# Kernel tuning notes

Measured on AMD Instinct MI355X. Metric: run time of the kernel, lower is better.

Reference implementation:

```python
import jax, jax.numpy as jnp
import numpy as np

N = 32768   # total nodes
P = 1024    # nodes per graph
B = 32      # graphs (N = B*P)
D = 256     # dim_h
H = 8       # num_heads
E = 262144  # edges
BN_EPS = 1e-5


def setup_inputs() -> dict:
    key = jax.random.key(0)
    ks = jax.random.split(key, 24)
    s = 0.05
    x = jax.random.normal(ks[0], (N, D), jnp.float32)
    src = jax.random.randint(ks[1], (E,), 0, N, dtype=jnp.int32)
    dst = (src // P) * P + jax.random.randint(ks[2], (E,), 0, P, dtype=jnp.int32)
    edge_index = jnp.stack([src, dst])  # [2, E], edges within the same graph
    edge_attr = jax.random.normal(ks[3], (E, D), jnp.float32)
    return {
        "x": x,
        "edge_index": edge_index,
        "edge_attr": edge_attr,
        # GINE nn: Linear(D,D) -> ReLU -> Linear(D,D)
        "gin_w1": s * jax.random.normal(ks[4], (D, D)),
        "gin_b1": jnp.zeros((D,)),
        "gin_w2": s * jax.random.normal(ks[5], (D, D)),
        "gin_b2": jnp.zeros((D,)),
        # MultiheadAttention packed in-proj and out-proj
        "in_w": s * jax.random.normal(ks[6], (3 * D, D)),
        "in_b": jnp.zeros((3 * D,)),
        "out_w": s * jax.random.normal(ks[7], (D, D)),
        "out_b": jnp.zeros((D,)),
        # BatchNorm1d affine params (training-mode batch stats)
        "bn1l_g": jnp.ones((D,)) + s * jax.random.normal(ks[8], (D,)),
        "bn1l_b": s * jax.random.normal(ks[9], (D,)),
        "bn1a_g": jnp.ones((D,)) + s * jax.random.normal(ks[10], (D,)),
        "bn1a_b": s * jax.random.normal(ks[11], (D,)),
        # FF block: Linear(D,2D) -> ReLU -> Linear(2D,D)
        "ff_w1": s * jax.random.normal(ks[12], (2 * D, D)),
        "ff_b1": jnp.zeros((2 * D,)),
        "ff_w2": s * jax.random.normal(ks[13], (D, 2 * D)),
        "ff_b2": jnp.zeros((D,)),
        "bn2_g": jnp.ones((D,)) + s * jax.random.normal(ks[14], (D,)),
        "bn2_b": s * jax.random.normal(ks[15], (D,)),
    }


def _batchnorm(x, g, b):
    # BatchNorm1d, training mode: biased batch statistics over the node axis.
    m = jnp.mean(x, axis=0)
    v = jnp.mean((x - m) ** 2, axis=0)
    return g * (x - m) * jax.lax.rsqrt(v + BN_EPS) + b


def reference(x, edge_index, edge_attr, gin_w1, gin_b1, gin_w2, gin_b2,
              in_w, in_b, out_w, out_b, bn1l_g, bn1l_b, bn1a_g, bn1a_b,
              ff_w1, ff_b1, ff_w2, ff_b2, bn2_g, bn2_b):
    h_in = x
    # ---- local branch: GINEConv (eps = 0) ----
    msg = jax.nn.relu(x[edge_index[0]] + edge_attr)          # [E, D]
    aggr = jax.ops.segment_sum(msg, edge_index[1], num_segments=N)
    z = x + aggr                                             # (1+eps)*x_i + sum msg
    h_local = jax.nn.relu(z @ gin_w1.T + gin_b1) @ gin_w2.T + gin_b2
    h_local = _batchnorm(h_in + h_local, bn1l_g, bn1l_b)
    # ---- global branch: dense-batch MHA (equal-size graphs -> full mask) ----
    hd = x.reshape(B, P, D)
    qkv = hd @ in_w.T + in_b                                 # [B, P, 3D]
    q, k, v = jnp.split(qkv, 3, axis=-1)
    dh = D // H
    q = q.reshape(B, P, H, dh).transpose(0, 2, 1, 3)         # [B, H, P, dh]
    k = k.reshape(B, P, H, dh).transpose(0, 2, 1, 3)
    v = v.reshape(B, P, H, dh).transpose(0, 2, 1, 3)
    scores = jnp.einsum("bhqd,bhkd->bhqk", q, k) / np.sqrt(dh)
    attn = jax.nn.softmax(scores, axis=-1)
    o = jnp.einsum("bhqk,bhkd->bhqd", attn, v)               # [B, H, P, dh]
    o = o.transpose(0, 2, 1, 3).reshape(B, P, D) @ out_w.T + out_b
    h_attn = o.reshape(N, D)
    h_attn = _batchnorm(h_in + h_attn, bn1a_g, bn1a_b)
    # ---- combine + FF + norm ----
    h = h_local + h_attn
    ff = jax.nn.relu(h @ ff_w1.T + ff_b1) @ ff_w2.T + ff_b2
    h = _batchnorm(h + ff, bn2_g, bn2_b)
    return h
```

## Files before the change

### kernel.cpp

```cpp
#include <hip/hip_runtime.h>
#include <hip/hip_bf16.h>

constexpr int D = 256;
constexpr int PG = 1024;

typedef __attribute__((ext_vector_type(8))) short bf16x8;
typedef __attribute__((ext_vector_type(4))) float f32x4;

__device__ inline short f2bf(float f) {
    __hip_bfloat16 h = __float2bfloat16(f);
    return *reinterpret_cast<short*>(&h);
}
__device__ inline float bf2f(short s) {
    return __uint_as_float(((unsigned)(unsigned short)s) << 16);
}

__global__ __launch_bounds__(256) void cvt_weights(
    const float* __restrict__ w1, const float* __restrict__ w2,
    const float* __restrict__ w3, const float* __restrict__ w4,
    const float* __restrict__ w5, const float* __restrict__ w6,
    short* __restrict__ out)
{
    int i = blockIdx.x * 256 + threadIdx.x;
    const float* src; int base;
    if (i < 16384)      { if (i < 8192) { src = w1; base = 0; }
                          else          { src = w2; base = 8192; } }
    else if (i < 40960) { src = w3; base = 16384; }
    else if (i < 49152) { src = w4; base = 40960; }
    else if (i < 65536) { src = w5; base = 49152; }
    else                { src = w6; base = 65536; }
    int k = i - base;
    float4 a = ((const float4*)src)[k * 2];
    float4 b = ((const float4*)src)[k * 2 + 1];
    bf16x8 v;
    v[0] = f2bf(a.x); v[1] = f2bf(a.y); v[2] = f2bf(a.z); v[3] = f2bf(a.w);
    v[4] = f2bf(b.x); v[5] = f2bf(b.y); v[6] = f2bf(b.z); v[7] = f2bf(b.w);
    ((bf16x8*)out)[i] = v;
}

__global__ __launch_bounds__(256) void hist_kernel(
    const int* __restrict__ dst, int* __restrict__ cnt, int E)
{
    int e = blockIdx.x * 256 + threadIdx.x;
    if (e < E) atomicAdd(&cnt[dst[e]], 1);
}

__global__ __launch_bounds__(256) void scan_block(
    const int* __restrict__ cnt, int* __restrict__ excl, int* __restrict__ bsum)
{
    __shared__ int sm[256];
    const int t = threadIdx.x;
    const int i = blockIdx.x * 256 + t;
    int v = cnt[i];
    sm[t] = v;
    __syncthreads();
    #pragma unroll
    for (int o = 1; o < 256; o <<= 1) {
        int u = (t >= o) ? sm[t - o] : 0;
        __syncthreads();
        sm[t] += u;
        __syncthreads();
    }
    excl[i] = sm[t] - v;
    if (t == 255) bsum[blockIdx.x] = sm[255];
}

__global__ __launch_bounds__(128) void scan_bsum(int* __restrict__ bsum)
{
    __shared__ int sm[128];
    const int t = threadIdx.x;
    int v = bsum[t];
    sm[t] = v;
    __syncthreads();
    #pragma unroll
    for (int o = 1; o < 128; o <<= 1) {
        int u = (t >= o) ? sm[t - o] : 0;
        __syncthreads();
        sm[t] += u;
        __syncthreads();
    }
    bsum[t] = sm[t] - v;
}

__global__ __launch_bounds__(256) void scan_add(
    const int* __restrict__ excl, const int* __restrict__ bsum,
    int* __restrict__ rowptr, int* __restrict__ ofs)
{
    int i = blockIdx.x * 256 + threadIdx.x;
    int r = excl[i] + bsum[blockIdx.x];
    rowptr[i] = r;
    ofs[i] = r;
}

__global__ __launch_bounds__(256) void scatter_kernel(
    const int* __restrict__ src, const int* __restrict__ dst,
    int* __restrict__ ofs, int* __restrict__ eord, int* __restrict__ esrc, int E)
{
    int e = blockIdx.x * 256 + threadIdx.x;
    if (e >= E) return;
    int d = dst[e];
    int pos = atomicAdd(&ofs[d], 1);
    eord[pos] = e;
    esrc[pos] = src[e];
}

__global__ __launch_bounds__(256) void csr_aggr(
    const float* __restrict__ x, const float* __restrict__ ea,
    const int* __restrict__ rowptr, const int* __restrict__ cnt,
    const int* __restrict__ eord, const int* __restrict__ esrc,
    short* __restrict__ z)
{
    int gid = blockIdx.x * 256 + threadIdx.x;
    int node = gid >> 6;
    int c = (gid & 63) << 2;
    int start = rowptr[node];
    int deg = cnt[node];
    float4 acc = *(const float4*)(x + (size_t)node * D + c);
    for (int i = 0; i < deg; ++i) {
        int e = eord[start + i];
        int s = esrc[start + i];
        float4 xa = *(const float4*)(x + (size_t)s * D + c);
        float4 av = *(const float4*)(ea + (size_t)e * D + c);
        acc.x += fmaxf(xa.x + av.x, 0.f);
        acc.y += fmaxf(xa.y + av.y, 0.f);
        acc.z += fmaxf(xa.z + av.z, 0.f);
        acc.w += fmaxf(xa.w + av.w, 0.f);
    }
    short4 r;
    r.x = f2bf(acc.x); r.y = f2bf(acc.y); r.z = f2bf(acc.z); r.w = f2bf(acc.w);
    *(short4*)(z + (size_t)node * D + c) = r;
}

template<bool XF32, bool RELU, bool ADDF, bool ADDB, bool STATS, bool SCALEQ>
__global__ __launch_bounds__(256) void gemm_mfma(
    const short* __restrict__ X, const float* __restrict__ Xf,
    const short* __restrict__ W, const float* __restrict__ bias,
    const float* __restrict__ addf, const short* __restrict__ addb,
    short* __restrict__ Y, float* __restrict__ st, int K, int M)
{
    __shared__ __align__(16) short Xs[128 * 72];
    __shared__ __align__(16) short Ws[128 * 72];

    const int nbx = gridDim.x;
    const int nwg = nbx * gridDim.y;
    const int bid = blockIdx.y * nbx + blockIdx.x;
    const int cpx = nwg >> 3;
    const int wg  = (bid & 7) * cpx + (bid >> 3);
    const int r0 = (wg / nbx) * 128;
    const int c0 = (wg % nbx) * 128;

    const int t = threadIdx.x, w = t >> 6, l = t & 63;
    const int wr = w >> 1, wc = w & 1, lg = l >> 4, lm = l & 15;
    const int srow = t >> 3;
    const int scol = (t & 7) * 8;

    f32x4 acc[4][4];
    #pragma unroll
    for (int i = 0; i < 4; ++i)
        #pragma unroll
        for (int j = 0; j < 4; ++j)
            acc[i][j] = (f32x4){0.f, 0.f, 0.f, 0.f};

    for (int k0 = 0; k0 < K; k0 += 64) {
        __syncthreads();
        #pragma unroll
        for (int it = 0; it < 4; ++it) {
            int r = it * 32 + srow;
            bf16x8 xv;
            if (XF32) {
                const float* p = Xf + (size_t)(r0 + r) * K + k0 + scol;
                float4 a = *(const float4*)p;
                float4 b = *(const float4*)(p + 4);
                xv[0] = f2bf(a.x); xv[1] = f2bf(a.y); xv[2] = f2bf(a.z); xv[3] = f2bf(a.w);
                xv[4] = f2bf(b.x); xv[5] = f2bf(b.y); xv[6] = f2bf(b.z); xv[7] = f2bf(b.w);
            } else {
                xv = *(const bf16x8*)(X + (size_t)(r0 + r) * K + k0 + scol);
            }
            bf16x8 wv = *(const bf16x8*)(W + (size_t)(c0 + r) * K + k0 + scol);
            *(bf16x8*)&Xs[r * 72 + scol] = xv;
            *(bf16x8*)&Ws[r * 72 + scol] = wv;
        }
        __syncthreads();

        bf16x8 af[4][2], bfr[4][2];
        #pragma unroll
        for (int i = 0; i < 4; ++i)
            #pragma unroll
            for (int ks = 0; ks < 2; ++ks) {
                af[i][ks]  = *(const bf16x8*)&Xs[(wr*64 + i*16 + lm)*72 + ks*32 + lg*8];
                bfr[i][ks] = *(const bf16x8*)&Ws[(wc*64 + i*16 + lm)*72 + ks*32 + lg*8];
            }
        #pragma unroll
        for (int i = 0; i < 4; ++i)
            #pragma unroll
            for (int j = 0; j < 4; ++j) {
                acc[i][j] = __builtin_amdgcn_mfma_f32_16x16x32_bf16(af[i][0], bfr[j][0], acc[i][j], 0, 0, 0);
                acc[i][j] = __builtin_amdgcn_mfma_f32_16x16x32_bf16(af[i][1], bfr[j][1], acc[i][j], 0, 0, 0);
            }
    }

    float s4[4] = {}, q4[4] = {};
    #pragma unroll
    for (int j = 0; j < 4; ++j) {
        int col = c0 + wc*64 + j*16 + lm;
        float bj = bias[col];
        #pragma unroll
        for (int i = 0; i < 4; ++i) {
            #pragma unroll
            for (int r = 0; r < 4; ++r) {
                int row = r0 + wr*64 + i*16 + lg*4 + r;
                size_t off = (size_t)row * M + col;
                float v = acc[i][j][r] + bj;
                if (RELU) v = fmaxf(v, 0.f);
                if (SCALEQ) { if (col < 256) v *= 0.17677669529663687f; }
                if (ADDF) v += addf[off];
                if (ADDB) v += bf2f(addb[off]);
                if (STATS) { s4[j] += v; q4[j] = fmaf(v, v, q4[j]); }
                Y[off] = f2bf(v);
            }
        }
    }
    if (STATS) {
        #pragma unroll
        for (int j = 0; j < 4; ++j) {
            s4[j] += __shfl_xor(s4[j], 16); q4[j] += __shfl_xor(q4[j], 16);
            s4[j] += __shfl_xor(s4[j], 32); q4[j] += __shfl_xor(q4[j], 32);
        }
        if (lg == 0) {
            #pragma unroll
            for (int j = 0; j < 4; ++j) {
                int col = c0 + wc*64 + j*16 + lm;
                atomicAdd(&st[col], s4[j]);
                atomicAdd(&st[256 + col], q4[j]);
            }
        }
    }
}

__global__ __launch_bounds__(256) void attn_mfma(
    const short* __restrict__ QKV, short* __restrict__ O)
{
    const int bh = blockIdx.x & 255;
    const int qblk = blockIdx.x >> 8;
    const int b = bh >> 3, h = bh & 7;
    const int t = threadIdx.x, w = t >> 6, l = t & 63;
    const int lg = l >> 4, lm = l & 15;
    const size_t gb = (size_t)b * PG * 768;
    const int q0 = qblk * 128 + w * 32;

    __shared__ __align__(16) short Ks[64 * 40];
    __shared__ __align__(16) short Vt[32 * 72];
    __shared__ __align__(16) short Ps[4][32 * 72];

    bf16x8 qa[2];
    #pragma unroll
    for (int qt = 0; qt < 2; ++qt)
        qa[qt] = *(const bf16x8*)(QKV + gb + (size_t)(q0 + qt*16 + lm) * 768 + h*32 + lg*8);

    f32x4 acc[2][2];
    #pragma unroll
    for (int qt = 0; qt < 2; ++qt)
        #pragma unroll
        for (int hf = 0; hf < 2; ++hf)
            acc[qt][hf] = (f32x4){0.f, 0.f, 0.f, 0.f};
    float lsum[2] = {0.f, 0.f};

    const int srow = t >> 2;
    const int sq = (t & 3) * 8;
    const short* Kb = QKV + gb + 256 + h*32 + sq;
    const short* Vb = QKV + gb + 512 + h*32 + sq;

    bf16x8 kreg = *(const bf16x8*)(Kb + (size_t)srow * 768);
    bf16x8 vreg = *(const bf16x8*)(Vb + (size_t)srow * 768);

    for (int kt = 0; kt < 16; ++kt) {
        *(bf16x8*)&Ks[srow * 40 + sq] = kreg;
        #pragma unroll
        for (int j = 0; j < 8; ++j) Vt[(sq + j) * 72 + srow] = vreg[j];
        __syncthreads();
        if (kt < 15) {
            kreg = *(const bf16x8*)(Kb + (size_t)((kt + 1) * 64 + srow) * 768);
            vreg = *(const bf16x8*)(Vb + (size_t)((kt + 1) * 64 + srow) * 768);
        }

        bf16x8 kf[4];
        #pragma unroll
        for (int s = 0; s < 4; ++s)
            kf[s] = *(const bf16x8*)&Ks[(s*16 + lm) * 40 + lg*8];

        #pragma unroll
        for (int qt = 0; qt < 2; ++qt) {
            #pragma unroll
            for (int s = 0; s < 4; ++s) {
                f32x4 c = (f32x4){0.f, 0.f, 0.f, 0.f};
                c = __builtin_amdgcn_mfma_f32_16x16x32_bf16(kf[s], qa[qt], c, 0, 0, 0);
                float p0 = __expf(c[0]), p1 = __expf(c[1]);
                float p2 = __expf(c[2]), p3 = __expf(c[3]);
                lsum[qt] += (p0 + p1) + (p2 + p3);
                short4 pk;
                pk.x = f2bf(p0); pk.y = f2bf(p1); pk.z = f2bf(p2); pk.w = f2bf(p3);
                *(short4*)&Ps[w][(qt*16 + lm) * 72 + s*16 + lg*4] = pk;
            }
        }

        bf16x8 vf[2][2];
        #pragma unroll
        for (int hf = 0; hf < 2; ++hf)
            #pragma unroll
            for (int g = 0; g < 2; ++g)
                vf[hf][g] = *(const bf16x8*)&Vt[(hf*16 + lm) * 72 + g*32 + lg*8];
        #pragma unroll
        for (int qt = 0; qt < 2; ++qt) {
            #pragma unroll
            for (int g = 0; g < 2; ++g) {
                bf16x8 pf = *(const bf16x8*)&Ps[w][(qt*16 + lm) * 72 + g*32 + lg*8];
                #pragma unroll
                for (int hf = 0; hf < 2; ++hf)
                    acc[qt][hf] = __builtin_amdgcn_mfma_f32_16x16x32_bf16(
                        pf, vf[hf][g], acc[qt][hf], 0, 0, 0);
            }
        }
        __syncthreads();
    }

    float red[2];
    #pragma unroll
    for (int qt = 0; qt < 2; ++qt) {
        float v = lsum[qt];
        v += __shfl_xor(v, 16);
        v += __shfl_xor(v, 32);
        red[qt] = 1.0f / v;
    }
    #pragma unroll
    for (int qt = 0; qt < 2; ++qt) {
        #pragma unroll
        for (int r = 0; r < 4; ++r) {
            float inv = __shfl(red[qt], lg*4 + r);
            int qrow = q0 + qt*16 + lg*4 + r;
            short* Op = O + ((size_t)b * PG + qrow) * D + h * 32;
            Op[lm]      = f2bf(acc[qt][0][r] * inv);
            Op[16 + lm] = f2bf(acc[qt][1][r] * inv);
        }
    }
}

__global__ __launch_bounds__(256) void bn_combine(
    const short* __restrict__ A, const short* __restrict__ Bq,
    const float* __restrict__ gl, const float* __restrict__ bl,
    const float* __restrict__ ga, const float* __restrict__ ba,
    const float* __restrict__ st, short* __restrict__ H, int n)
{
    const float invN = 1.0f / (float)n;
    size_t i = (size_t)blockIdx.x * 256 + threadIdx.x;
    int c0 = (int)((i & 31) << 3);
    bf16x8 av = ((const bf16x8*)A)[i];
    bf16x8 bv = ((const bf16x8*)Bq)[i];
    bf16x8 o;
    #pragma unroll
    for (int e = 0; e < 8; ++e) {
        int c = c0 + e;
        float m1 = st[c] * invN;
        float v1 = fmaxf(st[256 + c] * invN - m1 * m1, 0.f);
        float m2 = st[512 + c] * invN;
        float v2 = fmaxf(st[768 + c] * invN - m2 * m2, 0.f);
        float y1 = gl[c] * (bf2f(av[e]) - m1) * rsqrtf(v1 + 1e-5f) + bl[c];
        float y2 = ga[c] * (bf2f(bv[e]) - m2) * rsqrtf(v2 + 1e-5f) + ba[c];
        o[e] = f2bf(y1 + y2);
    }
    ((bf16x8*)H)[i] = o;
}

__global__ __launch_bounds__(256) void bn_apply(
    const short* __restrict__ X, const float* __restrict__ g,
    const float* __restrict__ bb, const float* __restrict__ st,
    float* __restrict__ out, int n)
{
    const float invN = 1.0f / (float)n;
    size_t i = (size_t)blockIdx.x * 256 + threadIdx.x;
    int c0 = (int)((i & 31) << 3);
    bf16x8 xv = ((const bf16x8*)X)[i];
    float r[8];
    #pragma unroll
    for (int e = 0; e < 8; ++e) {
        int c = c0 + e;
        float m = st[c] * invN;
        float v = fmaxf(st[256 + c] * invN - m * m, 0.f);
        r[e] = g[c] * (bf2f(xv[e]) - m) * rsqrtf(v + 1e-5f) + bb[c];
    }
    float4 o0 = {r[0], r[1], r[2], r[3]};
    float4 o1 = {r[4], r[5], r[6], r[7]};
    ((float4*)out)[i * 2]     = o0;
    ((float4*)out)[i * 2 + 1] = o1;
}

extern "C" void kernel_launch(void* const* d_in, const int* in_sizes, int n_in,
                              void* d_out, int out_size, void* d_ws, size_t ws_size,
                              hipStream_t stream)
{
    const float* x    = (const float*)d_in[0];
    const int*   ei   = (const int*)d_in[1];
    const float* ea   = (const float*)d_in[2];
    const float* gw1  = (const float*)d_in[3];
    const float* gb1  = (const float*)d_in[4];
    const float* gw2  = (const float*)d_in[5];
    const float* gb2  = (const float*)d_in[6];
    const float* inw  = (const float*)d_in[7];
    const float* inb  = (const float*)d_in[8];
    const float* outw = (const float*)d_in[9];
    const float* outb = (const float*)d_in[10];
    const float* g1l  = (const float*)d_in[11];
    const float* b1l  = (const float*)d_in[12];
    const float* g1a  = (const float*)d_in[13];
    const float* b1a  = (const float*)d_in[14];
    const float* fw1  = (const float*)d_in[15];
    const float* fb1  = (const float*)d_in[16];
    const float* fw2  = (const float*)d_in[17];
    const float* fb2  = (const float*)d_in[18];
    const float* g2   = (const float*)d_in[19];
    const float* b2   = (const float*)d_in[20];
    float* out = (float*)d_out;

    const int N = in_sizes[0] / D;
    const int E = in_sizes[1] / 2;
    const size_t ND = (size_t)N * D;

    short* Bp = (short*)d_ws;
    short* S0 = Bp;
    short* S1 = Bp + ND;
    short* S2 = Bp + 2 * ND;
    short* S3 = Bp + 3 * ND;
    short* S4 = Bp + 4 * ND;
    short* Wb = Bp + 5 * ND;
    short* gw1b = Wb, *gw2b = Wb + 65536, *inwb = Wb + 131072;
    short* outwb = Wb + 327680, *fw1b = Wb + 393216, *fw2b = Wb + 524288;
    float* st = (float*)(Wb + 655360);
    int* cnt    = (int*)(st + 1536);
    int* excl   = cnt + N;
    int* rowptr = excl + N;
    int* ofs    = rowptr + N;
    int* bsum   = ofs + N;
    int* eord   = bsum + 256;
    int* esrc   = eord + E;

    const int GR = N / 128;
    const int EB = (E + 255) / 256;

    cvt_weights<<<320, 256, 0, stream>>>(gw1, gw2, inw, outw, fw1, fw2, Wb);

    hipMemsetAsync(st, 0, (1536 + (size_t)N) * sizeof(int), stream);
    hist_kernel<<<EB, 256, 0, stream>>>(ei + E, cnt, E);
    scan_block<<<N / 256, 256, 0, stream>>>(cnt, excl, bsum);
    scan_bsum<<<1, 128, 0, stream>>>(bsum);
    scan_add<<<N / 256, 256, 0, stream>>>(excl, bsum, rowptr, ofs);
    scatter_kernel<<<EB, 256, 0, stream>>>(ei, ei + E, ofs, eord, esrc, E);

    csr_aggr<<<(N * 64) / 256, 256, 0, stream>>>(x, ea, rowptr, cnt, eord, esrc, S0);
    gemm_mfma<false, true , false, false, false, false><<<dim3(2, GR), 256, 0, stream>>>(
        S0, nullptr, gw1b, gb1, nullptr, nullptr, S1, nullptr, 256, 256);
    gemm_mfma<false, false, true , false, true , false><<<dim3(2, GR), 256, 0, stream>>>(
        S1, nullptr, gw2b, gb2, x, nullptr, S3, st, 256, 256);

    gemm_mfma<true , false, false, false, false, true ><<<dim3(6, GR), 256, 0, stream>>>(
        nullptr, x, inwb, inb, nullptr, nullptr, S0, nullptr, 256, 768);
    attn_mfma<<<(N / PG) * 8 * 8, 256, 0, stream>>>(S0, S4);
    gemm_mfma<false, false, true , false, true , false><<<dim3(2, GR), 256, 0, stream>>>(
        S4, nullptr, outwb, outb, x, nullptr, S0, st + 512, 256, 256);

    bn_combine<<<(unsigned)(ND / 8 / 256), 256, 0, stream>>>(
        S3, S0, g1l, b1l, g1a, b1a, st, S1, N);
    gemm_mfma<false, true , false, false, false, false><<<dim3(4, GR), 256, 0, stream>>>(
        S1, nullptr, fw1b, fb1, nullptr, nullptr, S2, nullptr, 256, 512);
    gemm_mfma<false, false, false, true , true , false><<<dim3(2, GR), 256, 0, stream>>>(
        S2, nullptr, fw2b, fb2, nullptr, S1, S4, st + 1024, 512, 256);
    bn_apply<<<(unsigned)(ND / 8 / 256), 256, 0, stream>>>(
        S4, g2, b2, st + 1024, out, N);
}
```

Baseline: 390.3 us.

## Transpose MFMA operands for vectorized GEMM stores; double-buffer K/V tiles in attention

Adds a TRANS template path that swaps the MFMA A/B operands, so each lane holds four consecutive output columns. The epilogue can then write short4 vectors and load the bias as float4, replacing scalar bf16 stores in the non-stats GEMMs. Attention now double-buffers the K and V shared-memory tiles, prefetching two tiles ahead and dropping one barrier per iteration. The cost is more shared memory and register pressure in attention. The TRANS path also omits the ADDF, ADDB and STATS handling, so it is only used where those are off.

Measured after the change: 400.6 us. +2.6%, slower.

```diff
diff --git a/kernel.cpp b/kernel.cpp
--- a/kernel.cpp
+++ b/kernel.cpp
@@ -131,7 +131,7 @@
     *(short4*)(z + (size_t)node * D + c) = r;
 }
 
-template<bool XF32, bool RELU, bool ADDF, bool ADDB, bool STATS, bool SCALEQ>
+template<bool XF32, bool RELU, bool ADDF, bool ADDB, bool STATS, bool SCALEQ, bool TRANS>
 __global__ __launch_bounds__(256) void gemm_mfma(
     const short* __restrict__ X, const float* __restrict__ Xf,
     const short* __restrict__ W, const float* __restrict__ bias,
@@ -194,44 +194,79 @@
         for (int i = 0; i < 4; ++i)
             #pragma unroll
             for (int j = 0; j < 4; ++j) {
-                acc[i][j] = __builtin_amdgcn_mfma_f32_16x16x32_bf16(af[i][0], bfr[j][0], acc[i][j], 0, 0, 0);
-                acc[i][j] = __builtin_amdgcn_mfma_f32_16x16x32_bf16(af[i][1], bfr[j][1], acc[i][j], 0, 0, 0);
-            }
-    }
-
-    float s4[4] = {}, q4[4] = {};
-    #pragma unroll
-    for (int j = 0; j < 4; ++j) {
-        int col = c0 + wc*64 + j*16 + lm;
-        float bj = bias[col];
+                if (TRANS) {
+                    acc[i][j] = __builtin_amdgcn_mfma_f32_16x16x32_bf16(bfr[j][0], af[i][0], acc[i][j], 0, 0, 0);
+                    acc[i][j] = __builtin_amdgcn_mfma_f32_16x16x32_bf16(bfr[j][1], af[i][1], acc[i][j], 0, 0, 0);
+                } else {
+                    acc[i][j] = __builtin_amdgcn_mfma_f32_16x16x32_bf16(af[i][0], bfr[j][0], acc[i][j], 0, 0, 0);
+                    acc[i][j] = __builtin_amdgcn_mfma_f32_16x16x32_bf16(af[i][1], bfr[j][1], acc[i][j], 0, 0, 0);
+                }
+            }
+    }
+
+    if (TRANS) {
         #pragma unroll
         for (int i = 0; i < 4; ++i) {
-            #pragma unroll
-            for (int r = 0; r < 4; ++r) {
-                int row = r0 + wr*64 + i*16 + lg*4 + r;
-                size_t off = (size_t)row * M + col;
-                float v = acc[i][j][r] + bj;
-                if (RELU) v = fmaxf(v, 0.f);
-                if (SCALEQ) { if (col < 256) v *= 0.17677669529663687f; }
-                if (ADDF) v += addf[off];
-                if (ADDB) v += bf2f(addb[off]);
-                if (STATS) { s4[j] += v; q4[j] = fmaf(v, v, q4[j]); }
-                Y[off] = f2bf(v);
-            }
-        }
-    }
-    if (STATS) {
+            int row = r0 + wr*64 + i*16 + lm;
+            #pragma unroll
+            for (int j = 0; j < 4; ++j) {
+                int col0 = c0 + wc*64 + j*16 + lg*4;
+                float4 bj = *(const float4*)(bias + col0);
+                size_t off = (size_t)row * M + col0;
+                float v0 = acc[i][j][0] + bj.x;
+                float v1 = acc[i][j][1] + bj.y;
+                float v2 = acc[i][j][2] + bj.z;
+                float v3 = acc[i][j][3] + bj.w;
+                if (RELU) {
+                    v0 = fmaxf(v0, 0.f); v1 = fmaxf(v1, 0.f);
+                    v2 = fmaxf(v2, 0.f); v3 = fmaxf(v3, 0.f);
+                }
+                if (SCALEQ) {
+                    if (col0 < 256) {
+                        const float rs = 0.17677669529663687f;
+                        v0 *= rs; v1 *= rs; v2 *= rs; v3 *= rs;
+                    }
+                }
+                short4 o;
+                o.x = f2bf(v0); o.y = f2bf(v1); o.z = f2bf(v2); o.w = f2bf(v3);
+                *(short4*)(Y + off) = o;
+            }
+        }
+    } else {
+        float s4[4] = {}, q4[4] = {};
         #pragma unroll
         for (int j = 0; j < 4; ++j) {
-            s4[j] += __shfl_xor(s4[j], 16); q4[j] += __shfl_xor(q4[j], 16);
-            s4[j] += __shfl_xor(s4[j], 32); q4[j] += __shfl_xor(q4[j], 32);
-        }
-        if (lg == 0) {
+            int col = c0 + wc*64 + j*16 + lm;
+            float bj = bias[col];
+            #pragma unroll
+            for (int i = 0; i < 4; ++i) {
+                #pragma unroll
+                for (int r = 0; r < 4; ++r) {
+                    int row = r0 + wr*64 + i*16 + lg*4 + r;
+                    size_t off = (size_t)row * M + col;
+                    float v = acc[i][j][r] + bj;
+                    if (RELU) v = fmaxf(v, 0.f);
+                    if (SCALEQ) { if (col < 256) v *= 0.17677669529663687f; }
+                    if (ADDF) v += addf[off];
+                    if (ADDB) v += bf2f(addb[off]);
+                    if (STATS) { s4[j] += v; q4[j] = fmaf(v, v, q4[j]); }
+                    Y[off] = f2bf(v);
+                }
+            }
+        }
+        if (STATS) {
             #pragma unroll
             for (int j = 0; j < 4; ++j) {
-                int col = c0 + wc*64 + j*16 + lm;
-                atomicAdd(&st[col], s4[j]);
-                atomicAdd(&st[256 + col], q4[j]);
+                s4[j] += __shfl_xor(s4[j], 16); q4[j] += __shfl_xor(q4[j], 16);
+                s4[j] += __shfl_xor(s4[j], 32); q4[j] += __shfl_xor(q4[j], 32);
+            }
+            if (lg == 0) {
+                #pragma unroll
+                for (int j = 0; j < 4; ++j) {
+                    int col = c0 + wc*64 + j*16 + lm;
+                    atomicAdd(&st[col], s4[j]);
+                    atomicAdd(&st[256 + col], q4[j]);
+                }
             }
         }
     }
@@ -248,8 +283,8 @@
     const size_t gb = (size_t)b * PG * 768;
     const int q0 = qblk * 128 + w * 32;
 
-    __shared__ __align__(16) short Ks[64 * 40];
-    __shared__ __align__(16) short Vt[32 * 72];
+    __shared__ __align__(16) short Ks[2][64 * 40];
+    __shared__ __align__(16) short Vt[2][32 * 72];
     __shared__ __align__(16) short Ps[4][32 * 72];
 
     bf16x8 qa[2];
@@ -272,21 +307,30 @@
 
     bf16x8 kreg = *(const bf16x8*)(Kb + (size_t)srow * 768);
     bf16x8 vreg = *(const bf16x8*)(Vb + (size_t)srow * 768);
+    *(bf16x8*)&Ks[0][srow * 40 + sq] = kreg;
+    #pragma unroll
+    for (int j = 0; j < 8; ++j) Vt[0][(sq + j) * 72 + srow] = vreg[j];
+    kreg = *(const bf16x8*)(Kb + (size_t)(64 + srow) * 768);
+    vreg = *(const bf16x8*)(Vb + (size_t)(64 + srow) * 768);
+    __syncthreads();
 
     for (int kt = 0; kt < 16; ++kt) {
-        *(bf16x8*)&Ks[srow * 40 + sq] = kreg;
-        #pragma unroll
-        for (int j = 0; j < 8; ++j) Vt[(sq + j) * 72 + srow] = vreg[j];
-        __syncthreads();
+        const int cur = kt & 1, nxt = cur ^ 1;
+
         if (kt < 15) {
-            kreg = *(const bf16x8*)(Kb + (size_t)((kt + 1) * 64 + srow) * 768);
-            vreg = *(const bf16x8*)(Vb + (size_t)((kt + 1) * 64 + srow) * 768);
+            *(bf16x8*)&Ks[nxt][srow * 40 + sq] = kreg;
+            #pragma unroll
+            for (int j = 0; j < 8; ++j) Vt[nxt][(sq + j) * 72 + srow] = vreg[j];
+        }
+        if (kt < 14) {
+            kreg = *(const bf16x8*)(Kb + (size_t)((kt + 2) * 64 + srow) * 768);
+            vreg = *(const bf16x8*)(Vb + (size_t)((kt + 2) * 64 + srow) * 768);
         }
 
         bf16x8 kf[4];
         #pragma unroll
         for (int s = 0; s < 4; ++s)
-            kf[s] = *(const bf16x8*)&Ks[(s*16 + lm) * 40 + lg*8];
+            kf[s] = *(const bf16x8*)&Ks[cur][(s*16 + lm) * 40 + lg*8];
 
         #pragma unroll
         for (int qt = 0; qt < 2; ++qt) {
@@ -308,7 +352,7 @@
         for (int hf = 0; hf < 2; ++hf)
             #pragma unroll
             for (int g = 0; g < 2; ++g)
-                vf[hf][g] = *(const bf16x8*)&Vt[(hf*16 + lm) * 72 + g*32 + lg*8];
+                vf[hf][g] = *(const bf16x8*)&Vt[cur][(hf*16 + lm) * 72 + g*32 + lg*8];
         #pragma unroll
         for (int qt = 0; qt < 2; ++qt) {
             #pragma unroll
@@ -455,22 +499,22 @@
     scatter_kernel<<<EB, 256, 0, stream>>>(ei, ei + E, ofs, eord, esrc, E);
 
     csr_aggr<<<(N * 64) / 256, 256, 0, stream>>>(x, ea, rowptr, cnt, eord, esrc, S0);
-    gemm_mfma<false, true , false, false, false, false><<<dim3(2, GR), 256, 0, stream>>>(
+    gemm_mfma<false, true , false, false, false, false, true ><<<dim3(2, GR), 256, 0, stream>>>(
         S0, nullptr, gw1b, gb1, nullptr, nullptr, S1, nullptr, 256, 256);
-    gemm_mfma<false, false, true , false, true , false><<<dim3(2, GR), 256, 0, stream>>>(
+    gemm_mfma<false, false, true , false, true , false, false><<<dim3(2, GR), 256, 0, stream>>>(
         S1, nullptr, gw2b, gb2, x, nullptr, S3, st, 256, 256);
 
-    gemm_mfma<true , false, false, false, false, true ><<<dim3(6, GR), 256, 0, stream>>>(
+    gemm_mfma<true , false, false, false, false, true , true ><<<dim3(6, GR), 256, 0, stream>>>(
         nullptr, x, inwb, inb, nullptr, nullptr, S0, nullptr, 256, 768);
     attn_mfma<<<(N / PG) * 8 * 8, 256, 0, stream>>>(S0, S4);
-    gemm_mfma<false, false, true , false, true , false><<<dim3(2, GR), 256, 0, stream>>>(
+    gemm_mfma<false, false, true , false, true , false, false><<<dim3(2, GR), 256, 0, stream>>>(
         S4, nullptr, outwb, outb, x, nullptr, S0, st + 512, 256, 256);
 
     bn_combine<<<(unsigned)(ND / 8 / 256), 256, 0, stream>>>(
         S3, S0, g1l, b1l, g1a, b1a, st, S1, N);
-    gemm_mfma<false, true , false, false, false, false><<<dim3(4, GR), 256, 0, stream>>>(
+    gemm_mfma<false, true , false, false, false, false, true ><<<dim3(4, GR), 256, 0, stream>>>(
         S1, nullptr, fw1b, fb1, nullptr, nullptr, S2, nullptr, 256, 512);
-    gemm_mfma<false, false, false, true , true , false><<<dim3(2, GR), 256, 0, stream>>>(
+    gemm_mfma<false, false, false, true , true , false, false><<<dim3(2, GR), 256, 0, stream>>>(
         S2, nullptr, fw2b, fb2, nullptr, S1, S4, st + 1024, 512, 256);
     bn_apply<<<(unsigned)(ND / 8 / 256), 256, 0, stream>>>(
         S4, g2, b2, st + 1024, out, N);
```

## Load GEMM tiles directly into LDS and pre-convert x to bf16

Applied to the files above, without the earlier changes.

The GEMM tile staging now uses global_load_lds (16-byte direct global-to-LDS loads) instead of loading through registers and then storing to LDS. Direct loads cannot convert data, so the fp32 in-projection input is no longer converted inside the GEMM; a new cvt_bf16 kernel converts x into a bf16 workspace buffer first. The LDS row padding is removed (stride 72 to 64) to fit the contiguous per-wave write layout of the direct load. This cuts register traffic and VGPR pressure in the load path, but risks LDS bank conflicts on the unpadded fragment reads, and it adds an extra kernel launch plus an extra bf16 buffer appended to the workspace.

After: 403.9 us. +3.5%, slower.

```diff
diff --git a/kernel.cpp b/kernel.cpp
--- a/kernel.cpp
+++ b/kernel.cpp
@@ -13,6 +13,23 @@
 }
 __device__ inline float bf2f(short s) {
     return __uint_as_float(((unsigned)(unsigned short)s) << 16);
+}
+__device__ inline void gl_lds16(const short* g, short* s) {
+    __builtin_amdgcn_global_load_lds(
+        (const __attribute__((address_space(1))) void*)g,
+        (__attribute__((address_space(3))) void*)s, 16, 0, 0);
+}
+
+__global__ __launch_bounds__(256) void cvt_bf16(
+    const float* __restrict__ X, short* __restrict__ Y)
+{
+    int i = blockIdx.x * 256 + threadIdx.x;
+    float4 a = ((const float4*)X)[i * 2];
+    float4 b = ((const float4*)X)[i * 2 + 1];
+    bf16x8 v;
+    v[0] = f2bf(a.x); v[1] = f2bf(a.y); v[2] = f2bf(a.z); v[3] = f2bf(a.w);
+    v[4] = f2bf(b.x); v[5] = f2bf(b.y); v[6] = f2bf(b.z); v[7] = f2bf(b.w);
+    ((bf16x8*)Y)[i] = v;
 }
 
 __global__ __launch_bounds__(256) void cvt_weights(
@@ -131,15 +148,15 @@
     *(short4*)(z + (size_t)node * D + c) = r;
 }
 
-template<bool XF32, bool RELU, bool ADDF, bool ADDB, bool STATS, bool SCALEQ>
+template<bool RELU, bool ADDF, bool ADDB, bool STATS, bool SCALEQ>
 __global__ __launch_bounds__(256) void gemm_mfma(
-    const short* __restrict__ X, const float* __restrict__ Xf,
-    const short* __restrict__ W, const float* __restrict__ bias,
+    const short* __restrict__ X, const short* __restrict__ W,
+    const float* __restrict__ bias,
     const float* __restrict__ addf, const short* __restrict__ addb,
     short* __restrict__ Y, float* __restrict__ st, int K, int M)
 {
-    __shared__ __align__(16) short Xs[128 * 72];
-    __shared__ __align__(16) short Ws[128 * 72];
+    __shared__ __align__(16) short Xs[128 * 64];
+    __shared__ __align__(16) short Ws[128 * 64];
 
     const int nbx = gridDim.x;
     const int nwg = nbx * gridDim.y;
@@ -151,8 +168,8 @@
 
     const int t = threadIdx.x, w = t >> 6, l = t & 63;
     const int wr = w >> 1, wc = w & 1, lg = l >> 4, lm = l & 15;
-    const int srow = t >> 3;
-    const int scol = (t & 7) * 8;
+    const int srl = l >> 3;
+    const int scol = (l & 7) * 8;
 
     f32x4 acc[4][4];
     #pragma unroll
@@ -165,20 +182,9 @@
         __syncthreads();
         #pragma unroll
         for (int it = 0; it < 4; ++it) {
-            int r = it * 32 + srow;
-            bf16x8 xv;
-            if (XF32) {
-                const float* p = Xf + (size_t)(r0 + r) * K + k0 + scol;
-                float4 a = *(const float4*)p;
-                float4 b = *(const float4*)(p + 4);
-                xv[0] = f2bf(a.x); xv[1] = f2bf(a.y); xv[2] = f2bf(a.z); xv[3] = f2bf(a.w);
-                xv[4] = f2bf(b.x); xv[5] = f2bf(b.y); xv[6] = f2bf(b.z); xv[7] = f2bf(b.w);
-            } else {
-                xv = *(const bf16x8*)(X + (size_t)(r0 + r) * K + k0 + scol);
-            }
-            bf16x8 wv = *(const bf16x8*)(W + (size_t)(c0 + r) * K + k0 + scol);
-            *(bf16x8*)&Xs[r * 72 + scol] = xv;
-            *(bf16x8*)&Ws[r * 72 + scol] = wv;
+            int r = w * 32 + it * 8;
+            gl_lds16(X + (size_t)(r0 + r + srl) * K + k0 + scol, &Xs[r * 64]);
+            gl_lds16(W + (size_t)(c0 + r + srl) * K + k0 + scol, &Ws[r * 64]);
         }
         __syncthreads();
 
@@ -187,8 +193,8 @@
         for (int i = 0; i < 4; ++i)
             #pragma unroll
             for (int ks = 0; ks < 2; ++ks) {
-                af[i][ks]  = *(const bf16x8*)&Xs[(wr*64 + i*16 + lm)*72 + ks*32 + lg*8];
-                bfr[i][ks] = *(const bf16x8*)&Ws[(wc*64 + i*16 + lm)*72 + ks*32 + lg*8];
+                af[i][ks]  = *(const bf16x8*)&Xs[(wr*64 + i*16 + lm)*64 + ks*32 + lg*8];
+                bfr[i][ks] = *(const bf16x8*)&Ws[(wc*64 + i*16 + lm)*64 + ks*32 + lg*8];
             }
         #pragma unroll
         for (int i = 0; i < 4; ++i)
@@ -441,10 +447,12 @@
     int* bsum   = ofs + N;
     int* eord   = bsum + 256;
     int* esrc   = eord + E;
+    short* xb   = (short*)(esrc + E);
 
     const int GR = N / 128;
     const int EB = (E + 255) / 256;
 
+    cvt_bf16<<<(unsigned)(ND / 8 / 256), 256, 0, stream>>>(x, xb);
     cvt_weights<<<320, 256, 0, stream>>>(gw1, gw2, inw, outw, fw1, fw2, Wb);
 
     hipMemsetAsync(st, 0, (1536 + (size_t)N) * sizeof(int), stream);
@@ -455,23 +463,23 @@
     scatter_kernel<<<EB, 256, 0, stream>>>(ei, ei + E, ofs, eord, esrc, E);
 
     csr_aggr<<<(N * 64) / 256, 256, 0, stream>>>(x, ea, rowptr, cnt, eord, esrc, S0);
-    gemm_mfma<false, true , false, false, false, false><<<dim3(2, GR), 256, 0, stream>>>(
-        S0, nullptr, gw1b, gb1, nullptr, nullptr, S1, nullptr, 256, 256);
-    gemm_mfma<false, false, true , false, true , false><<<dim3(2, GR), 256, 0, stream>>>(
-        S1, nullptr, gw2b, gb2, x, nullptr, S3, st, 256, 256);
-
-    gemm_mfma<true , false, false, false, false, true ><<<dim3(6, GR), 256, 0, stream>>>(
-        nullptr, x, inwb, inb, nullptr, nullptr, S0, nullptr, 256, 768);
+    gemm_mfma<true , false, false, false, false><<<dim3(2, GR), 256, 0, stream>>>(
+        S0, gw1b, gb1, nullptr, nullptr, S1, nullptr, 256, 256);
+    gemm_mfma<false, true , false, true , false><<<dim3(2, GR), 256, 0, stream>>>(
+        S1, gw2b, gb2, x, nullptr, S3, st, 256, 256);
+
+    gemm_mfma<false, false, false, false, true ><<<dim3(6, GR), 256, 0, stream>>>(
+        xb, inwb, inb, nullptr, nullptr, S0, nullptr, 256, 768);
     attn_mfma<<<(N / PG) * 8 * 8, 256, 0, stream>>>(S0, S4);
-    gemm_mfma<false, false, true , false, true , false><<<dim3(2, GR), 256, 0, stream>>>(
-        S4, nullptr, outwb, outb, x, nullptr, S0, st + 512, 256, 256);
+    gemm_mfma<false, true , false, true , false><<<dim3(2, GR), 256, 0, stream>>>(
+        S4, outwb, outb, x, nullptr, S0, st + 512, 256, 256);
 
     bn_combine<<<(unsigned)(ND / 8 / 256), 256, 0, stream>>>(
         S3, S0, g1l, b1l, g1a, b1a, st, S1, N);
-    gemm_mfma<false, true , false, false, false, false><<<dim3(4, GR), 256, 0, stream>>>(
-        S1, nullptr, fw1b, fb1, nullptr, nullptr, S2, nullptr, 256, 512);
-    gemm_mfma<false, false, false, true , true , false><<<dim3(2, GR), 256, 0, stream>>>(
-        S2, nullptr, fw2b, fb2, nullptr, S1, S4, st + 1024, 512, 256);
+    gemm_mfma<true , false, false, false, false><<<dim3(4, GR), 256, 0, stream>>>(
+        S1, fw1b, fb1, nullptr, nullptr, S2, nullptr, 256, 512);
+    gemm_mfma<false, false, true , true , false><<<dim3(2, GR), 256, 0, stream>>>(
+        S2, fw2b, fb2, nullptr, S1, S4, st + 1024, 512, 256);
     bn_apply<<<(unsigned)(ND / 8 / 256), 256, 0, stream>>>(
         S4, g2, b2, st + 1024, out, N);
 }
```
